# Performance work log

Measured on AMD Instinct MI355X. Metric: run time of the kernel, lower is better.

## Reference

```python
import jax, jax.numpy as jnp
import numpy as np

H = 1024   # hdim
D = 200    # linear_first bottleneck (fixed in source)
K = 8      # len(token_ids)
B = 8
L = 4096


def setup_inputs() -> dict:
    key = jax.random.key(0)
    ks = jax.random.split(key, 7)
    hidd_states = jax.random.normal(ks[0], (B, L, H), dtype=jnp.float32)
    prompt_types = jax.random.randint(ks[1], (B,), 0, 3, dtype=jnp.int32)
    ner_labels = jax.random.randint(ks[2], (B, L), 0, K, dtype=jnp.int32)
    # learned params (PyTorch Linear default-ish init scale)
    W1 = jax.random.normal(ks[3], (H, D), dtype=jnp.float32) / np.sqrt(H)
    b1 = jnp.zeros((D,), dtype=jnp.float32)
    W2 = jax.random.normal(ks[4], (D, K), dtype=jnp.float32) / np.sqrt(D)
    b2 = jnp.zeros((K,), dtype=jnp.float32)
    return {"hidd_states": hidd_states, "W1": W1, "b1": b1, "W2": W2,
            "b2": b2, "prompt_types": prompt_types, "ner_labels": ner_labels}


def _det_output(hidd, W1, b1, W2, b2, prompt_types):
    # hidd: [B, L, H]
    # attn = linear_second(tanh(linear_first(h)))  -> [B, L, K]
    attn = jnp.tanh(jnp.einsum('blh,hd->bld', hidd, W1) + b1)
    attn = jnp.einsum('bld,dk->blk', attn, W2) + b2
    # bmm(attn[:, :, None], h[:, None, :]).mean(dim=2) == attn * mean_h(h)
    m = jnp.mean(hidd, axis=-1)            # [B, L]
    s = attn * m[..., None]                # [B, L, K]
    Lf = s.shape[1]
    # prefix: running mean over t <= j
    pre = jnp.cumsum(s, axis=1) / jnp.arange(1, Lf + 1, dtype=s.dtype)[:, None]
    # postfix: running mean over t >= j (reverse cumsum)
    rev = jnp.flip(jnp.cumsum(jnp.flip(s, axis=1), axis=1), axis=1)
    post = rev / (Lf - jnp.arange(Lf, dtype=s.dtype))[:, None]
    # other: per-token, no mean over dim 0
    pt = prompt_types[:, None, None]
    det = jnp.where(pt == 0, pre, jnp.where(pt == 1, post, s))  # [B, L, K]
    return det


def reference(hidd_states, W1, b1, W2, b2, prompt_types, ner_labels):
    det = _det_output(hidd_states, W1, b1, W2, b2, prompt_types)
    ner_preds = jax.nn.softmax(det, axis=-1)                     # [B, L, K]
    # CrossEntropyLoss applied (as in the repo) to the softmax probs:
    logp = jax.nn.log_softmax(ner_preds, axis=-1)                # [B, L, K]
    picked = jnp.take_along_axis(logp, ner_labels[..., None].astype(jnp.int32), axis=-1)[..., 0]
    losses = -jnp.mean(picked, axis=1)                           # [B]
    return losses
```

## Files before the change

kernel.cpp:

```cpp
#include <hip/hip_runtime.h>
#include <hip/hip_bf16.h>
#include <math.h>

#define H   1024
#define Dd  200
#define Kc  8
#define Bb  8
#define Ll  4096
#define Mm  (Bb*Ll)

typedef __attribute__((ext_vector_type(8))) short short8;
typedef __attribute__((ext_vector_type(4))) float f32x4;

#define OFF_W1T  0
#define OFF_S    425984
#define OFF_SEG  (OFF_S + Mm*Kc*4)
#define OFF_PART (OFF_SEG + Bb*16*Kc*4)
#define WS_NEEDED (OFF_PART + 128*4)

#define GLOAD16(g, l) __builtin_amdgcn_global_load_lds( \
    (const __attribute__((address_space(1))) void*)(g),  \
    (__attribute__((address_space(3))) void*)(l), 16, 0, 0)

__device__ __forceinline__ unsigned short f2bf(float x){
  unsigned u = __float_as_uint(x);
  unsigned r = (u + 0x7FFFu + ((u >> 16) & 1u)) >> 16;
  return (unsigned short)r;
}

union Uc { short8 s8; __hip_bfloat162 h2[4]; };

__global__ __launch_bounds__(256) void prep_w1t(const float* __restrict__ W1,
                                                unsigned short* __restrict__ W1T){
  int idx = blockIdx.x * 256 + threadIdx.x;
  int d = idx >> 10;
  int h = idx & 1023;
  float v = (d < Dd) ? W1[h * Dd + d] : 0.f;
  W1T[idx] = f2bf(v);
}

__global__ __launch_bounds__(512) __attribute__((amdgpu_waves_per_eu(4)))
void gemm_fused(const float* __restrict__ hidd,
                const unsigned short* __restrict__ W1T,
                const float* __restrict__ b1,
                const float* __restrict__ W2,
                const float* __restrict__ b2,
                float* __restrict__ sOut){
  __shared__ char lA[64 * 128];
  __shared__ char lB[2 * 32768];
  __shared__ float epart[8][4][4][8];
  __shared__ float lrow[64];
  char* lAc = lA;

  const int tid  = threadIdx.x;
  const int lane = tid & 63;
  const int wid  = tid >> 6;
  const int lc   = lane & 15;
  const int lg   = lane >> 4;
  const int wr   = wid >> 1;
  const int wc   = wid & 1;
  const int t0   = wc * 7;
  const int ntw  = 7 - wc;
  const long rowBase = (long)blockIdx.x * 64;

  const int arow = tid >> 3, ak8 = tid & 7;
  const float* ag = hidd + (size_t)(rowBase + arow) * H + ak8 * 8;
  const int awb = ((arow * 128 + ak8 * 16) ^ ((arow & 7) << 4));

  const int swz = (((lane & 7) ^ (lane >> 3)) & 7) * 16;
  const char* bsrcj[4];
  #pragma unroll
  for (int j = 0; j < 4; ++j){
    int colj = wid * 32 + j * 8 + (lane >> 3);
    colj = (colj < 207) ? colj : 207;
    bsrcj[j] = (const char*)W1T + (size_t)colj * 2048 + swz;
  }

  const int acs   = (lc & 7) << 4;
  const int aoff0 = (wr * 16 + lc) * 128 + ((lg * 16) ^ acs);
  const int aoff1 = (wr * 16 + lc) * 128 + (((64 + lg * 16)) ^ acs);

  int boff0[7], boff1[7];
  #pragma unroll
  for (int tt = 0; tt < 7; ++tt){
    const int col = (t0 + tt) * 16 + lc;
    const int cs  = (col & 7) * 16;
    boff0[tt] = col * 128 + ((lg * 16) ^ cs);
    boff1[tt] = col * 128 + ((64 + lg * 16) ^ cs);
  }

  float4 pf[2][2];
  pf[0][0] = *(const float4*)(ag);
  pf[0][1] = *(const float4*)(ag + 4);
  #pragma unroll
  for (int j = 0; j < 4; ++j)
    GLOAD16(bsrcj[j], &lB[wid * 4096 + j * 1024]);

  f32x4 acc[7];
  #pragma unroll
  for (int t = 0; t < 7; ++t) acc[t] = (f32x4){0.f, 0.f, 0.f, 0.f};
  float ms = 0.f;

#define GEMM_STEP(KT, CUR, NXT) do {                                           \
    if ((KT) < 15){                                                            \
      pf[NXT][0] = *(const float4*)(ag + ((KT) + 1) * 64);                     \
      pf[NXT][1] = *(const float4*)(ag + ((KT) + 1) * 64 + 4);                 \
      GLOAD16(bsrcj[0] + ((KT)+1)*128, &lB[(NXT)*32768 + wid*4096 + 0*1024]);  \
      GLOAD16(bsrcj[1] + ((KT)+1)*128, &lB[(NXT)*32768 + wid*4096 + 1*1024]);  \
      GLOAD16(bsrcj[2] + ((KT)+1)*128, &lB[(NXT)*32768 + wid*4096 + 2*1024]);  \
      GLOAD16(bsrcj[3] + ((KT)+1)*128, &lB[(NXT)*32768 + wid*4096 + 3*1024]);  \
      asm volatile("s_waitcnt vmcnt(6)" ::: "memory");                         \
    } else {                                                                   \
      asm volatile("s_waitcnt vmcnt(0)" ::: "memory");                         \
    }                                                                          \
    {                                                                          \
      const float4 a0 = pf[CUR][0], a1 = pf[CUR][1];                           \
      ms += a0.x + a0.y + a0.z + a0.w + a1.x + a1.y + a1.z + a1.w;             \
      Uc u;                                                                    \
      u.h2[0] = __float22bfloat162_rn(make_float2(a0.x, a0.y));                \
      u.h2[1] = __float22bfloat162_rn(make_float2(a0.z, a0.w));                \
      u.h2[2] = __float22bfloat162_rn(make_float2(a1.x, a1.y));                \
      u.h2[3] = __float22bfloat162_rn(make_float2(a1.z, a1.w));                \
      *(short8*)(lAc + awb) = u.s8;                                            \
    }                                                                          \
    asm volatile("s_waitcnt lgkmcnt(0)" ::: "memory");                         \
    __builtin_amdgcn_s_barrier();                                              \
    __builtin_amdgcn_sched_barrier(0);                                         \
    {                                                                          \
      const short8 af0 = *(const short8*)(lAc + aoff0);                        \
      const short8 af1 = *(const short8*)(lAc + aoff1);                        \
      const char* bb = &lB[(CUR) * 32768];                                     \
      _Pragma("unroll")                                                        \
      for (int tt = 0; tt < 7; ++tt){                                          \
        if (tt < ntw){                                                         \
          const short8 bf0 = *(const short8*)(bb + boff0[tt]);                 \
          const short8 bf1 = *(const short8*)(bb + boff1[tt]);                 \
          acc[tt] = __builtin_amdgcn_mfma_f32_16x16x32_bf16(af0, bf0, acc[tt], 0, 0, 0); \
          acc[tt] = __builtin_amdgcn_mfma_f32_16x16x32_bf16(af1, bf1, acc[tt], 0, 0, 0); \
        }                                                                      \
      }                                                                        \
    }                                                                          \
    if ((KT) < 15){                                                            \
      __builtin_amdgcn_sched_barrier(0);                                       \
      __builtin_amdgcn_s_barrier();                                            \
      __builtin_amdgcn_sched_barrier(0);                                       \
    }                                                                          \
  } while (0)

  for (int m = 0; m < 8; ++m){
    const int kt0 = m * 2;
    GEMM_STEP(kt0, 0, 1);
    GEMM_STEP(kt0 + 1, 1, 0);
  }
#undef GEMM_STEP

  ms += __shfl_xor(ms, 1); ms += __shfl_xor(ms, 2); ms += __shfl_xor(ms, 4);
  if ((tid & 7) == 0) lrow[tid >> 3] = ms * (1.0f / 1024.0f);

  float part[4][Kc];
  #pragma unroll
  for (int r = 0; r < 4; ++r)
    #pragma unroll
    for (int k = 0; k < Kc; ++k) part[r][k] = 0.f;

  #pragma unroll
  for (int tt = 0; tt < 7; ++tt){
    if (tt < ntw){
      const int col = (t0 + tt) * 16 + lc;
      float b1v = 0.f;
      float w2v[Kc];
      if (col < Dd){
        b1v = b1[col];
        const float4 wa = *(const float4*)(W2 + col * Kc);
        const float4 wb = *(const float4*)(W2 + col * Kc + 4);
        w2v[0] = wa.x; w2v[1] = wa.y; w2v[2] = wa.z; w2v[3] = wa.w;
        w2v[4] = wb.x; w2v[5] = wb.y; w2v[6] = wb.z; w2v[7] = wb.w;
      } else {
        #pragma unroll
        for (int k = 0; k < Kc; ++k) w2v[k] = 0.f;
      }
      #pragma unroll
      for (int r = 0; r < 4; ++r){
        const float a = tanhf(acc[tt][r] + b1v);
        #pragma unroll
        for (int k = 0; k < Kc; ++k) part[r][k] = fmaf(a, w2v[k], part[r][k]);
      }
    }
  }
  #pragma unroll
  for (int m = 1; m < 16; m <<= 1){
    #pragma unroll
    for (int r = 0; r < 4; ++r)
      #pragma unroll
      for (int k = 0; k < Kc; ++k)
        part[r][k] += __shfl_xor(part[r][k], m);
  }
  if ((lane & 15) == 0){
    #pragma unroll
    for (int r = 0; r < 4; ++r)
      #pragma unroll
      for (int k = 0; k < Kc; ++k)
        epart[wid][lg][r][k] = part[r][k];
  }
  __syncthreads();

  {
    const int row2 = tid >> 3, k = tid & 7;
    const int wr2 = row2 >> 4, lg2 = (row2 >> 2) & 3, r2 = row2 & 3;
    const float v = epart[wr2 * 2][lg2][r2][k] + epart[wr2 * 2 + 1][lg2][r2][k];
    sOut[(size_t)(rowBase + row2) * Kc + k] = (v + b2[k]) * lrow[row2];
  }
}

__global__ __launch_bounds__(256) void seg_sum(const float* __restrict__ s,
                                               float* __restrict__ segs){
  int b   = blockIdx.x >> 4;
  int seg = blockIdx.x & 15;
  int tid = threadIdx.x, lane = tid & 63, wid = tid >> 6;
  int l = seg * 256 + tid;
  const float4* sp = (const float4*)(s + ((long)(b * Ll + l)) * Kc);
  float4 v0 = sp[0], v1 = sp[1];
  float v[8] = {v0.x, v0.y, v0.z, v0.w, v1.x, v1.y, v1.z, v1.w};
  #pragma unroll
  for (int k = 0; k < 8; ++k){
    float x = v[k];
    x += __shfl_xor(x, 1);  x += __shfl_xor(x, 2);  x += __shfl_xor(x, 4);
    x += __shfl_xor(x, 8);  x += __shfl_xor(x, 16); x += __shfl_xor(x, 32);
    v[k] = x;
  }
  __shared__ float part[4][8];
  if (lane == 0){
    #pragma unroll
    for (int k = 0; k < 8; ++k) part[wid][k] = v[k];
  }
  __syncthreads();
  if (tid < 8){
    float t = part[0][tid] + part[1][tid] + part[2][tid] + part[3][tid];
    segs[(b * 16 + seg) * 8 + tid] = t;
  }
}

__global__ __launch_bounds__(256) void scan_loss(const float* __restrict__ s,
                                                 const float* __restrict__ segs,
                                                 const int* __restrict__ ptypes,
                                                 const int* __restrict__ labels,
                                                 float* __restrict__ partial){
  int b   = blockIdx.x >> 4;
  int seg = blockIdx.x & 15;
  int tid = threadIdx.x, lane = tid & 63, wid = tid >> 6;
  int l = seg * 256 + tid;

  float carry[8], T[8];
  #pragma unroll
  for (int k = 0; k < 8; ++k){ carry[k] = 0.f; T[k] = 0.f; }
  for (int ss = 0; ss < 16; ++ss){
    #pragma unroll
    for (int k = 0; k < 8; ++k){
      float x = segs[(b * 16 + ss) * 8 + k];
      T[k] += x;
      if (ss < seg) carry[k] += x;
    }
  }

  const float4* sp = (const float4*)(s + ((long)(b * Ll + l)) * Kc);
  float4 v0 = sp[0], v1 = sp[1];
  float sv[8] = {v0.x, v0.y, v0.z, v0.w, v1.x, v1.y, v1.z, v1.w};
  float P[8];
  #pragma unroll
  for (int k = 0; k < 8; ++k) P[k] = sv[k];

  #pragma unroll
  for (int st = 1; st < 64; st <<= 1){
    #pragma unroll
    for (int k = 0; k < 8; ++k){
      float u = __shfl_up(P[k], st);
      if (lane >= st) P[k] += u;
    }
  }
  __shared__ float wsum[4][8];
  if (lane == 63){
    #pragma unroll
    for (int k = 0; k < 8; ++k) wsum[wid][k] = P[k];
  }
  __syncthreads();
  for (int w = 0; w < wid; ++w){
    #pragma unroll
    for (int k = 0; k < 8; ++k) P[k] += wsum[w][k];
  }
  #pragma unroll
  for (int k = 0; k < 8; ++k) P[k] += carry[k];

  int pt = ptypes[b];
  float det[8];
  if (pt == 0){
    float inv = 1.0f / (float)(l + 1);
    #pragma unroll
    for (int k = 0; k < 8; ++k) det[k] = P[k] * inv;
  } else if (pt == 1){
    float inv = 1.0f / (float)(Ll - l);
    #pragma unroll
    for (int k = 0; k < 8; ++k) det[k] = (T[k] - P[k] + sv[k]) * inv;
  } else {
    #pragma unroll
    for (int k = 0; k < 8; ++k) det[k] = sv[k];
  }

  float mx = det[0];
  #pragma unroll
  for (int k = 1; k < 8; ++k) mx = fmaxf(mx, det[k]);
  float e[8], Z = 0.f;
  #pragma unroll
  for (int k = 0; k < 8; ++k){ e[k] = expf(det[k] - mx); Z += e[k]; }
  float invZ = 1.0f / Z;
  float p[8];
  #pragma unroll
  for (int k = 0; k < 8; ++k) p[k] = e[k] * invZ;
  float mx2 = p[0];
  #pragma unroll
  for (int k = 1; k < 8; ++k) mx2 = fmaxf(mx2, p[k]);
  float Z2 = 0.f;
  #pragma unroll
  for (int k = 0; k < 8; ++k) Z2 += expf(p[k] - mx2);
  float lse = logf(Z2) + mx2;

  int lab = labels[b * Ll + l];
  float picked = 0.f;
  #pragma unroll
  for (int k = 0; k < 8; ++k) picked = (lab == k) ? (p[k] - lse) : picked;

  float a = picked;
  a += __shfl_xor(a, 1);  a += __shfl_xor(a, 2);  a += __shfl_xor(a, 4);
  a += __shfl_xor(a, 8);  a += __shfl_xor(a, 16); a += __shfl_xor(a, 32);
  __shared__ float red[4];
  if (lane == 0) red[wid] = a;
  __syncthreads();
  if (tid == 0){
    partial[blockIdx.x] = red[0] + red[1] + red[2] + red[3];
  }
}

__global__ __launch_bounds__(128) void final_loss(const float* __restrict__ partial,
                                                  float* __restrict__ out){
  int tid = threadIdx.x;
  float v = partial[tid];
  v += __shfl_xor(v, 1); v += __shfl_xor(v, 2);
  v += __shfl_xor(v, 4); v += __shfl_xor(v, 8);
  if ((tid & 15) == 0) out[tid >> 4] = -v * (1.0f / (float)Ll);
}

extern "C" void kernel_launch(void* const* d_in, const int* in_sizes, int n_in,
                              void* d_out, int out_size, void* d_ws, size_t ws_size,
                              hipStream_t stream){
  const float* hidd  = (const float*)d_in[0];
  const float* W1    = (const float*)d_in[1];
  const float* b1    = (const float*)d_in[2];
  const float* W2    = (const float*)d_in[3];
  const float* b2    = (const float*)d_in[4];
  const int* ptypes  = (const int*)d_in[5];
  const int* labels  = (const int*)d_in[6];
  float* out = (float*)d_out;
  char* ws = (char*)d_ws;
  if (ws_size < (size_t)WS_NEEDED) return;

  unsigned short* W1T = (unsigned short*)(ws + OFF_W1T);
  float* s       = (float*)(ws + OFF_S);
  float* segs    = (float*)(ws + OFF_SEG);
  float* partial = (float*)(ws + OFF_PART);

  prep_w1t<<<(208 * H) / 256, 256, 0, stream>>>(W1, W1T);
  gemm_fused<<<Mm / 64, 512, 0, stream>>>(hidd, W1T, b1, W2, b2, s);
  seg_sum<<<Bb * 16, 256, 0, stream>>>(s, segs);
  scan_loss<<<Bb * 16, 256, 0, stream>>>(s, segs, ptypes, labels, partial);
  final_loss<<<1, 128, 0, stream>>>(partial, out);
}
```

Measured before the change: 229.9 us.

## Restructure GEMM wave tiling, fuse segment sums, tile W1 transpose

The GEMM warp mapping changes from a 4x2 split (7 N-tiles per wave, one A fragment) to teams that each own two row groups and 3-4 N-tiles, so every B fragment feeds two MFMAs and LDS traffic per MFMA drops. The separate seg_sum kernel is removed: the GEMM epilogue reduces each block's 64 rows and atomically adds them into the per-segment sums, which a memset now zeroes. The W1 transpose kernel uses an LDS-tiled transpose with vectorised loads and stores, and W1T is padded to 256 columns so the GEMM no longer clamps column indices. The epilogue reuses LDS buffers, adding an extra barrier, and the atomics make the float summation order nondeterministic.

```diff
diff --git a/kernel.cpp b/kernel.cpp
--- a/kernel.cpp
+++ b/kernel.cpp
@@ -13,7 +13,7 @@
 typedef __attribute__((ext_vector_type(4))) float f32x4;
 
 #define OFF_W1T  0
-#define OFF_S    425984
+#define OFF_S    524288
 #define OFF_SEG  (OFF_S + Mm*Kc*4)
 #define OFF_PART (OFF_SEG + Bb*16*Kc*4)
 #define WS_NEEDED (OFF_PART + 128*4)
@@ -32,35 +32,68 @@
 
 __global__ __launch_bounds__(256) void prep_w1t(const float* __restrict__ W1,
                                                 unsigned short* __restrict__ W1T){
-  int idx = blockIdx.x * 256 + threadIdx.x;
-  int d = idx >> 10;
-  int h = idx & 1023;
-  float v = (d < Dd) ? W1[h * Dd + d] : 0.f;
-  W1T[idx] = f2bf(v);
-}
-
-__global__ __launch_bounds__(512) __attribute__((amdgpu_waves_per_eu(4)))
+  __shared__ unsigned short lt[64][72];
+  const int bd = blockIdx.x & 3;
+  const int bh = blockIdx.x >> 2;
+  const int d0 = bd * 64, h0 = bh * 64;
+  const int t  = threadIdx.x;
+
+  const int hr = t >> 2, dc = (t & 3) * 16;
+  #pragma unroll
+  for (int dd = 0; dd < 4; ++dd){
+    const int d = d0 + dc + dd * 4;
+    float x0 = 0.f, x1 = 0.f, x2 = 0.f, x3 = 0.f;
+    if (d + 3 < Dd){
+      const float4 v = *(const float4*)(W1 + (size_t)(h0 + hr) * Dd + d);
+      x0 = v.x; x1 = v.y; x2 = v.z; x3 = v.w;
+    } else {
+      if (d + 0 < Dd) x0 = W1[(size_t)(h0 + hr) * Dd + d + 0];
+      if (d + 1 < Dd) x1 = W1[(size_t)(h0 + hr) * Dd + d + 1];
+      if (d + 2 < Dd) x2 = W1[(size_t)(h0 + hr) * Dd + d + 2];
+      if (d + 3 < Dd) x3 = W1[(size_t)(h0 + hr) * Dd + d + 3];
+    }
+    ushort4 p; p.x = f2bf(x0); p.y = f2bf(x1); p.z = f2bf(x2); p.w = f2bf(x3);
+    *(ushort4*)(&lt[hr][dc + dd * 4]) = p;
+  }
+  __syncthreads();
+
+  const int dl = t >> 2, hc = (t & 3) * 16;
+  #pragma unroll
+  for (int j = 0; j < 4; ++j){
+    ushort4 o;
+    o.x = lt[hc + j * 4 + 0][dl];
+    o.y = lt[hc + j * 4 + 1][dl];
+    o.z = lt[hc + j * 4 + 2][dl];
+    o.w = lt[hc + j * 4 + 3][dl];
+    *(ushort4*)(W1T + (size_t)(d0 + dl) * H + h0 + hc + j * 4) = o;
+  }
+}
+
+__global__ __launch_bounds__(512) __attribute__((amdgpu_waves_per_eu(4, 4)))
 void gemm_fused(const float* __restrict__ hidd,
                 const unsigned short* __restrict__ W1T,
                 const float* __restrict__ b1,
                 const float* __restrict__ W2,
                 const float* __restrict__ b2,
-                float* __restrict__ sOut){
-  __shared__ char lA[64 * 128];
+                float* __restrict__ sOut,
+                float* __restrict__ segs){
+  __shared__ char lA[8192];
   __shared__ char lB[2 * 32768];
-  __shared__ float epart[8][4][4][8];
-  __shared__ float lrow[64];
   char* lAc = lA;
+  float* epart = (float*)lA;
+  float* lrow  = (float*)lB;
+  float* red2  = (float*)(lB + 256);
+#define EP(w, rg, g, r, k) ((((((w)*2+(rg))*4+(g))*4+(r))*8)+(k))
 
   const int tid  = threadIdx.x;
   const int lane = tid & 63;
   const int wid  = tid >> 6;
   const int lc   = lane & 15;
   const int lg   = lane >> 4;
-  const int wr   = wid >> 1;
-  const int wc   = wid & 1;
-  const int t0   = wc * 7;
-  const int ntw  = 7 - wc;
+  const int team = wid & 3;
+  const int rgp  = wid >> 2;
+  const int tBase = (team == 0) ? 0 : (team == 1) ? 4 : (team == 2) ? 7 : 10;
+  const int tCnt  = (team == 0) ? 4 : 3;
   const long rowBase = (long)blockIdx.x * 64;
 
   const int arow = tid >> 3, ak8 = tid & 7;
@@ -71,22 +104,23 @@
   const char* bsrcj[4];
   #pragma unroll
   for (int j = 0; j < 4; ++j){
-    int colj = wid * 32 + j * 8 + (lane >> 3);
-    colj = (colj < 207) ? colj : 207;
+    const int colj = wid * 32 + j * 8 + (lane >> 3);
     bsrcj[j] = (const char*)W1T + (size_t)colj * 2048 + swz;
   }
 
-  const int acs   = (lc & 7) << 4;
-  const int aoff0 = (wr * 16 + lc) * 128 + ((lg * 16) ^ acs);
-  const int aoff1 = (wr * 16 + lc) * 128 + (((64 + lg * 16)) ^ acs);
-
-  int boff0[7], boff1[7];
-  #pragma unroll
-  for (int tt = 0; tt < 7; ++tt){
-    const int col = (t0 + tt) * 16 + lc;
-    const int cs  = (col & 7) * 16;
-    boff0[tt] = col * 128 + ((lg * 16) ^ cs);
-    boff1[tt] = col * 128 + ((64 + lg * 16) ^ cs);
+  int aoff[2][2], boff[4][2];
+  #pragma unroll
+  for (int rg = 0; rg < 2; ++rg){
+    const int rowA = rgp * 32 + rg * 16 + lc;
+    aoff[rg][0] = rowA * 128 + (((lg * 16)) ^ ((lc & 7) << 4));
+    aoff[rg][1] = rowA * 128 + ((64 + lg * 16) ^ ((lc & 7) << 4));
+  }
+  #pragma unroll
+  for (int tt = 0; tt < 4; ++tt){
+    const int tEff = tBase + ((tt < tCnt) ? tt : 0);
+    const int col  = tEff * 16 + lc;
+    boff[tt][0] = col * 128 + (((lg * 16)) ^ ((lc & 7) << 4));
+    boff[tt][1] = col * 128 + ((64 + lg * 16) ^ ((lc & 7) << 4));
   }
 
   float4 pf[2][2];
@@ -96,9 +130,11 @@
   for (int j = 0; j < 4; ++j)
     GLOAD16(bsrcj[j], &lB[wid * 4096 + j * 1024]);
 
-  f32x4 acc[7];
-  #pragma unroll
-  for (int t = 0; t < 7; ++t) acc[t] = (f32x4){0.f, 0.f, 0.f, 0.f};
+  f32x4 acc[2][4];
+  #pragma unroll
+  for (int rg = 0; rg < 2; ++rg)
+    #pragma unroll
+    for (int tt = 0; tt < 4; ++tt) acc[rg][tt] = (f32x4){0.f, 0.f, 0.f, 0.f};
   float ms = 0.f;
 
 #define GEMM_STEP(KT, CUR, NXT) do {                                           \
@@ -127,16 +163,18 @@
     __builtin_amdgcn_s_barrier();                                              \
     __builtin_amdgcn_sched_barrier(0);                                         \
     {                                                                          \
-      const short8 af0 = *(const short8*)(lAc + aoff0);                        \
-      const short8 af1 = *(const short8*)(lAc + aoff1);                        \
       const char* bb = &lB[(CUR) * 32768];                                     \
       _Pragma("unroll")                                                        \
-      for (int tt = 0; tt < 7; ++tt){                                          \
-        if (tt < ntw){                                                         \
-          const short8 bf0 = *(const short8*)(bb + boff0[tt]);                 \
-          const short8 bf1 = *(const short8*)(bb + boff1[tt]);                 \
-          acc[tt] = __builtin_amdgcn_mfma_f32_16x16x32_bf16(af0, bf0, acc[tt], 0, 0, 0); \
-          acc[tt] = __builtin_amdgcn_mfma_f32_16x16x32_bf16(af1, bf1, acc[tt], 0, 0, 0); \
+      for (int h = 0; h < 2; ++h){                                             \
+        const short8 aF0 = *(const short8*)(lAc + aoff[0][h]);                 \
+        const short8 aF1 = *(const short8*)(lAc + aoff[1][h]);                 \
+        _Pragma("unroll")                                                      \
+        for (int tt = 0; tt < 4; ++tt){                                        \
+          if (tt < tCnt){                                                      \
+            const short8 bF = *(const short8*)(bb + boff[tt][h]);              \
+            acc[0][tt] = __builtin_amdgcn_mfma_f32_16x16x32_bf16(aF0, bF, acc[0][tt], 0, 0, 0); \
+            acc[1][tt] = __builtin_amdgcn_mfma_f32_16x16x32_bf16(aF1, bF, acc[1][tt], 0, 0, 0); \
+          }                                                                    \
         }                                                                      \
       }                                                                        \
     }                                                                          \
@@ -154,90 +192,84 @@
   }
 #undef GEMM_STEP
 
+  __syncthreads();
+
   ms += __shfl_xor(ms, 1); ms += __shfl_xor(ms, 2); ms += __shfl_xor(ms, 4);
   if ((tid & 7) == 0) lrow[tid >> 3] = ms * (1.0f / 1024.0f);
 
-  float part[4][Kc];
-  #pragma unroll
-  for (int r = 0; r < 4; ++r)
-    #pragma unroll
-    for (int k = 0; k < Kc; ++k) part[r][k] = 0.f;
-
-  #pragma unroll
-  for (int tt = 0; tt < 7; ++tt){
-    if (tt < ntw){
-      const int col = (t0 + tt) * 16 + lc;
-      float b1v = 0.f;
-      float w2v[Kc];
-      if (col < Dd){
-        b1v = b1[col];
-        const float4 wa = *(const float4*)(W2 + col * Kc);
-        const float4 wb = *(const float4*)(W2 + col * Kc + 4);
-        w2v[0] = wa.x; w2v[1] = wa.y; w2v[2] = wa.z; w2v[3] = wa.w;
-        w2v[4] = wb.x; w2v[5] = wb.y; w2v[6] = wb.z; w2v[7] = wb.w;
-      } else {
-        #pragma unroll
-        for (int k = 0; k < Kc; ++k) w2v[k] = 0.f;
-      }
-      #pragma unroll
-      for (int r = 0; r < 4; ++r){
-        const float a = tanhf(acc[tt][r] + b1v);
-        #pragma unroll
-        for (int k = 0; k < Kc; ++k) part[r][k] = fmaf(a, w2v[k], part[r][k]);
-      }
-    }
-  }
-  #pragma unroll
-  for (int m = 1; m < 16; m <<= 1){
+  #pragma unroll
+  for (int rg = 0; rg < 2; ++rg){
+    float part[4][Kc];
     #pragma unroll
     for (int r = 0; r < 4; ++r)
       #pragma unroll
-      for (int k = 0; k < Kc; ++k)
-        part[r][k] += __shfl_xor(part[r][k], m);
-  }
-  if ((lane & 15) == 0){
-    #pragma unroll
-    for (int r = 0; r < 4; ++r)
+      for (int k = 0; k < Kc; ++k) part[r][k] = 0.f;
+
+    #pragma unroll
+    for (int tt = 0; tt < 4; ++tt){
+      if (tt < tCnt){
+        const int col = (tBase + tt) * 16 + lc;
+        float b1v = 0.f;
+        float w2v[Kc];
+        if (col < Dd){
+          b1v = b1[col];
+          const float4 wa = *(const float4*)(W2 + col * Kc);
+          const float4 wb = *(const float4*)(W2 + col * Kc + 4);
+          w2v[0] = wa.x; w2v[1] = wa.y; w2v[2] = wa.z; w2v[3] = wa.w;
+          w2v[4] = wb.x; w2v[5] = wb.y; w2v[6] = wb.z; w2v[7] = wb.w;
+        } else {
+          #pragma unroll
+          for (int k = 0; k < Kc; ++k) w2v[k] = 0.f;
+        }
+        #pragma unroll
+        for (int r = 0; r < 4; ++r){
+          const float a = tanhf(acc[rg][tt][r] + b1v);
+          #pragma unroll
+          for (int k = 0; k < Kc; ++k) part[r][k] = fmaf(a, w2v[k], part[r][k]);
+        }
+      }
+    }
+    #pragma unroll
+    for (int m = 1; m < 16; m <<= 1){
       #pragma unroll
-      for (int k = 0; k < Kc; ++k)
-        epart[wid][lg][r][k] = part[r][k];
+      for (int r = 0; r < 4; ++r)
+        #pragma unroll
+        for (int k = 0; k < Kc; ++k)
+          part[r][k] += __shfl_xor(part[r][k], m);
+    }
+    if (lc == 0){
+      #pragma unroll
+      for (int r = 0; r < 4; ++r)
+        #pragma unroll
+        for (int k = 0; k < Kc; ++k)
+          epart[EP(wid, rg, lg, r, k)] = part[r][k];
+    }
   }
   __syncthreads();
 
   {
     const int row2 = tid >> 3, k = tid & 7;
-    const int wr2 = row2 >> 4, lg2 = (row2 >> 2) & 3, r2 = row2 & 3;
-    const float v = epart[wr2 * 2][lg2][r2][k] + epart[wr2 * 2 + 1][lg2][r2][k];
-    sOut[(size_t)(rowBase + row2) * Kc + k] = (v + b2[k]) * lrow[row2];
-  }
-}
-
-__global__ __launch_bounds__(256) void seg_sum(const float* __restrict__ s,
-                                               float* __restrict__ segs){
-  int b   = blockIdx.x >> 4;
-  int seg = blockIdx.x & 15;
-  int tid = threadIdx.x, lane = tid & 63, wid = tid >> 6;
-  int l = seg * 256 + tid;
-  const float4* sp = (const float4*)(s + ((long)(b * Ll + l)) * Kc);
-  float4 v0 = sp[0], v1 = sp[1];
-  float v[8] = {v0.x, v0.y, v0.z, v0.w, v1.x, v1.y, v1.z, v1.w};
-  #pragma unroll
-  for (int k = 0; k < 8; ++k){
-    float x = v[k];
-    x += __shfl_xor(x, 1);  x += __shfl_xor(x, 2);  x += __shfl_xor(x, 4);
-    x += __shfl_xor(x, 8);  x += __shfl_xor(x, 16); x += __shfl_xor(x, 32);
-    v[k] = x;
-  }
-  __shared__ float part[4][8];
-  if (lane == 0){
-    #pragma unroll
-    for (int k = 0; k < 8; ++k) part[wid][k] = v[k];
+    const int rgp2 = row2 >> 5, rg2 = (row2 >> 4) & 1;
+    const int lg2 = (row2 >> 2) & 3, r2 = row2 & 3;
+    float v = 0.f;
+    #pragma unroll
+    for (int tm = 0; tm < 4; ++tm)
+      v += epart[EP(rgp2 * 4 + tm, rg2, lg2, r2, k)];
+    const float sv = (v + b2[k]) * lrow[row2];
+    sOut[(size_t)(rowBase + row2) * Kc + k] = sv;
+
+    float x = sv;
+    x += __shfl_xor(x, 8); x += __shfl_xor(x, 16); x += __shfl_xor(x, 32);
+    if (lane < 8) red2[wid * 8 + lane] = x;
   }
   __syncthreads();
   if (tid < 8){
-    float t = part[0][tid] + part[1][tid] + part[2][tid] + part[3][tid];
-    segs[(b * 16 + seg) * 8 + tid] = t;
-  }
+    float t = 0.f;
+    #pragma unroll
+    for (int w = 0; w < 8; ++w) t += red2[w * 8 + tid];
+    atomicAdd(segs + (rowBase >> 8) * 8 + tid, t);
+  }
+#undef EP
 }
 
 __global__ __launch_bounds__(256) void scan_loss(const float* __restrict__ s,
@@ -367,9 +399,9 @@
   float* segs    = (float*)(ws + OFF_SEG);
   float* partial = (float*)(ws + OFF_PART);
 
-  prep_w1t<<<(208 * H) / 256, 256, 0, stream>>>(W1, W1T);
-  gemm_fused<<<Mm / 64, 512, 0, stream>>>(hidd, W1T, b1, W2, b2, s);
-  seg_sum<<<Bb * 16, 256, 0, stream>>>(s, segs);
+  prep_w1t<<<64, 256, 0, stream>>>(W1, W1T);
+  hipMemsetAsync(segs, 0, Bb * 16 * Kc * sizeof(float), stream);
+  gemm_fused<<<Mm / 64, 512, 0, stream>>>(hidd, W1T, b1, W2, b2, s, segs);
   scan_loss<<<Bb * 16, 256, 0, stream>>>(s, segs, ptypes, labels, partial);
   final_loss<<<1, 128, 0, stream>>>(partial, out);
 }
```

After: 237.1 us. +3.1%, slower.
